# Kernel optimization log

Hardware: AMD Instinct MI355X
Metric: run time of the kernel (lower is better)

The kernel has to match this reference:

```python
import jax, jax.numpy as jnp
import numpy as np

STRIDES = (2, 2, 1)   # module init arg: (2,2,1) per docstring example
EPS = 1e-5            # InstanceNorm epsilon
ALPHA = 0.2           # leaky relu slope
DN = ('NDHWC', 'DHWIO', 'NDHWC')


def setup_inputs() -> dict:
    key = jax.random.key(0)
    k1, k2 = jax.random.split(key, 2)
    # x: [B, D, H, W, Cin] NDHWC volume batch
    x = jax.random.normal(k1, (4, 128, 128, 32, 32), dtype=jnp.float32)
    # w: per-sample hypernetwork kernels [B, kD, kH, kW, Cin, Cout]
    w = jax.random.normal(k2, (4, 3, 3, 3, 32, 64), dtype=jnp.float32) * 0.05
    # InstanceNorm affine params (learned)
    gamma = jnp.ones((64,), dtype=jnp.float32)
    beta = jnp.zeros((64,), dtype=jnp.float32)
    return {"x": x, "w": w, "gamma": gamma, "beta": beta}


def _per_sample_conv(xi, wi):
    # xi: [D,H,W,Cin], wi: [kD,kH,kW,Cin,Cout] -> [D',H',W',Cout]
    return jax.lax.conv_general_dilated(
        xi[None], wi, window_strides=STRIDES, padding='SAME',
        dimension_numbers=DN)[0]


def reference(x, w, gamma, beta):
    # batched dynamic conv: distinct kernel per sample, vectorized via vmap
    y = jax.vmap(_per_sample_conv)(x, w)          # [B, D', H', W', Cout]
    # InstanceNorm: normalize over spatial dims per sample, per channel
    mu = jnp.mean(y, axis=(1, 2, 3), keepdims=True)
    var = jnp.var(y, axis=(1, 2, 3), keepdims=True)
    y = (y - mu) * jax.lax.rsqrt(var + EPS) * gamma + beta
    # leaky relu alpha=0.2
    return jnp.where(y >= 0, y, ALPHA * y)
```

## Files before the change

### kernel.cpp

```cpp
#include <hip/hip_runtime.h>

#define B_ 4
#define D_ 128
#define H_ 128
#define W_ 32
#define CI 32
#define CO 64
#define OD 64
#define OH 64
#define OW 32
#define S_SPATIAL (OD*OH*OW)
#define EPS 1e-5f
#define ALPHA 0.2f

#define XR 9
#define XC 34
#define XUNITS (4*XR*XC)

typedef __attribute__((ext_vector_type(8))) short short8;
typedef __attribute__((ext_vector_type(4))) float f32x4;

__device__ inline short f2bf(float f) {
    union { float f; unsigned u; } v; v.f = f;
    unsigned r = v.u + 0x7FFFu + ((v.u >> 16) & 1u);
    return (short)(r >> 16);
}

__device__ inline short8 pack8(float4 a, float4 b) {
    short8 r;
    r[0]=f2bf(a.x); r[1]=f2bf(a.y); r[2]=f2bf(a.z); r[3]=f2bf(a.w);
    r[4]=f2bf(b.x); r[5]=f2bf(b.y); r[6]=f2bf(b.z); r[7]=f2bf(b.w);
    return r;
}

__global__ __launch_bounds__(512) void zero_ws_kernel(float* ws) {
    ws[threadIdx.x] = 0.f;
}

__global__ __launch_bounds__(64) void wprep_kernel(const float* __restrict__ w,
                                                   short* __restrict__ wp) {
    int blk = blockIdx.x;
    int nf  = blk & 3;
    int tb  = blk >> 2;
    int l   = threadIdx.x;
    int l15 = l & 15, lhi = l >> 4;
    const float* wsrc = w + (size_t)tb * (CI*CO);
    short8 v;
#pragma unroll
    for (int j = 0; j < 8; ++j)
        v[j] = f2bf(wsrc[(lhi*8 + j)*CO + nf*16 + l15]);
    *(short8*)(wp + (size_t)blk*512 + l*8) = v;
}

__global__ __launch_bounds__(256) void conv_mfma_kernel(const float* __restrict__ x,
                                                        const short* __restrict__ wp,
                                                        float* __restrict__ out,
                                                        float* __restrict__ ws) {
    const int bid = blockIdx.x;
    const int b   = bid >> 10;
    const int od  = (bid >> 4) & 63;
    const int oh0 = (bid & 15) << 2;
    const int t   = threadIdx.x;
    const int wv  = t >> 6;
    const int l   = t & 63;
    const int l15 = l & 15;
    const int lhi = l >> 4;

    const float* xb  = x + (size_t)b * (D_*H_*W_*CI);
    const short* wpb = wp + (size_t)b * (27*2048);

    __shared__ short xlds[XUNITS*8];
    __shared__ float lsum[4][64];
    __shared__ float lsq[4][64];

    f32x4 acc[2][4];
#pragma unroll
    for (int mf = 0; mf < 2; ++mf)
#pragma unroll
        for (int nf = 0; nf < 4; ++nf)
            acc[mf][nf] = (f32x4){0.f, 0.f, 0.f, 0.f};

    for (int kd = 0; kd < 3; ++kd) {
        const int id = od*2 + kd;
        if (id >= D_) break;
        const float* xsl = xb + (size_t)id * (H_*W_*CI);

        __syncthreads();
        for (int u = t; u < XUNITS; u += 256) {
            int c  = u % XC;
            int rc = u / XC;
            int r  = rc % XR;
            int g  = rc / XR;
            int ih = oh0*2 + r;
            int iw = c - 1;
            short8 v = (short8){0,0,0,0,0,0,0,0};
            if (ih < H_ && (unsigned)iw < (unsigned)W_) {
                const float* p = xsl + (size_t)ih*(W_*CI) + iw*CI + g*8;
                v = pack8(*(const float4*)p, *(const float4*)(p + 4));
            }
            *(short8*)(xlds + (size_t)u*8) = v;
        }
        __syncthreads();

        const short* wkd = wpb + (size_t)kd*(9*2048) + l*8;
#pragma unroll
        for (int kh = 0; kh < 3; ++kh) {
#pragma unroll
            for (int kw = 0; kw < 3; ++kw) {
                const short* wpt = wkd + (kh*3 + kw)*2048;
                short8 bf0 = *(const short8*)(wpt);
                short8 bf1 = *(const short8*)(wpt + 512);
                short8 bf2 = *(const short8*)(wpt + 1024);
                short8 bf3 = *(const short8*)(wpt + 1536);
                const int r = 2*wv + kh;
#pragma unroll
                for (int mf = 0; mf < 2; ++mf) {
                    int c = mf*16 + l15 + kw;
                    short8 a = *(const short8*)(xlds + (((lhi*XR + r)*XC + c) * 8));
                    acc[mf][0] = __builtin_amdgcn_mfma_f32_16x16x32_bf16(a, bf0, acc[mf][0], 0,0,0);
                    acc[mf][1] = __builtin_amdgcn_mfma_f32_16x16x32_bf16(a, bf1, acc[mf][1], 0,0,0);
                    acc[mf][2] = __builtin_amdgcn_mfma_f32_16x16x32_bf16(a, bf2, acc[mf][2], 0,0,0);
                    acc[mf][3] = __builtin_amdgcn_mfma_f32_16x16x32_bf16(a, bf3, acc[mf][3], 0,0,0);
                }
            }
        }
    }

    const int oh = oh0 + wv;
    float* yb = out + (size_t)((b*OD + od)*OH + oh) * (OW*CO);
#pragma unroll
    for (int mf = 0; mf < 2; ++mf)
#pragma unroll
        for (int nf = 0; nf < 4; ++nf)
#pragma unroll
            for (int r = 0; r < 4; ++r) {
                int ow = mf*16 + lhi*4 + r;
                int co = nf*16 + l15;
                yb[ow*CO + co] = acc[mf][nf][r];
            }

    float csum[4], csq[4];
#pragma unroll
    for (int nf = 0; nf < 4; ++nf) {
        float s = 0.f, q = 0.f;
#pragma unroll
        for (int mf = 0; mf < 2; ++mf)
#pragma unroll
            for (int r = 0; r < 4; ++r) {
                float v = acc[mf][nf][r];
                s += v;
                q = fmaf(v, v, q);
            }
        s += __shfl_xor(s, 16, 64); s += __shfl_xor(s, 32, 64);
        q += __shfl_xor(q, 16, 64); q += __shfl_xor(q, 32, 64);
        csum[nf] = s; csq[nf] = q;
    }
    if (lhi == 0) {
#pragma unroll
        for (int nf = 0; nf < 4; ++nf) {
            lsum[wv][nf*16 + l15] = csum[nf];
            lsq[wv][nf*16 + l15]  = csq[nf];
        }
    }
    __syncthreads();
    if (t < 64) {
        float s = lsum[0][t] + lsum[1][t] + lsum[2][t] + lsum[3][t];
        float q = lsq[0][t]  + lsq[1][t]  + lsq[2][t]  + lsq[3][t];
        atomicAdd(&ws[b*64 + t], s);
        atomicAdd(&ws[256 + b*64 + t], q);
    }
}

__global__ __launch_bounds__(256) void finalize_kernel(float* ws,
                                                       const float* __restrict__ gamma,
                                                       const float* __restrict__ beta) {
    int t = threadIdx.x;
    int co = t & 63;
    const float invS = 1.0f / (float)S_SPATIAL;
    float sum = ws[t];
    float sq  = ws[256 + t];
    float mu  = sum * invS;
    float var = sq * invS - mu*mu;
    float scale = rsqrtf(var + EPS) * gamma[co];
    ws[512 + t] = scale;
    ws[768 + t] = beta[co] - mu*scale;
}

__global__ __launch_bounds__(256) void norm_kernel(float* __restrict__ y,
                                                   const float* __restrict__ ws) {
    size_t i = (size_t)blockIdx.x * 256 + threadIdx.x;
    int b = (int)(i >> 21);
    const float4* scp = (const float4*)(ws + 512 + b*64);
    const float4* shp = (const float4*)(ws + 768 + b*64);
    float4 sc = scp[i & 15];
    float4 sh = shp[i & 15];
    float4 v = ((const float4*)y)[i];
    float4 r;
    r.x = fmaf(v.x, sc.x, sh.x);
    r.y = fmaf(v.y, sc.y, sh.y);
    r.z = fmaf(v.z, sc.z, sh.z);
    r.w = fmaf(v.w, sc.w, sh.w);
    r.x = r.x >= 0.f ? r.x : ALPHA * r.x;
    r.y = r.y >= 0.f ? r.y : ALPHA * r.y;
    r.z = r.z >= 0.f ? r.z : ALPHA * r.z;
    r.w = r.w >= 0.f ? r.w : ALPHA * r.w;
    ((float4*)y)[i] = r;
}

extern "C" void kernel_launch(void* const* d_in, const int* in_sizes, int n_in,
                              void* d_out, int out_size, void* d_ws, size_t ws_size,
                              hipStream_t stream) {
    const float* x     = (const float*)d_in[0];
    const float* w     = (const float*)d_in[1];
    const float* gamma = (const float*)d_in[2];
    const float* beta  = (const float*)d_in[3];
    float* out = (float*)d_out;
    float* ws  = (float*)d_ws;
    short* wp  = (short*)((char*)d_ws + 4096);

    zero_ws_kernel<<<1, 512, 0, stream>>>(ws);
    wprep_kernel<<<B_*27*4, 64, 0, stream>>>(w, wp);
    conv_mfma_kernel<<<B_*OD*(OH/4), 256, 0, stream>>>(x, wp, out, ws);
    finalize_kernel<<<1, 256, 0, stream>>>(ws, gamma, beta);
    norm_kernel<<<32768, 256, 0, stream>>>(out, ws);
}
```

Measured before the change: 239.7 us.

## Stage input slices asynchronously into LDS with double buffering

Replaces the synchronous per-slice global load, bf16 conversion and LDS store with direct global-to-LDS async loads of raw fp32 rows into two swizzled buffers. Loading the next depth slice overlaps with MFMA compute on the current one, and conversion to bf16 moves into the compute loop. Padding is handled by clamping addresses and masking fragments instead of zero-filled halo storage. The cost is doubled LDS use (fp32, two buffers) and repeated per-fragment conversion work, with occupancy hinted at 2 blocks.

```diff
diff --git a/kernel.cpp b/kernel.cpp
--- a/kernel.cpp
+++ b/kernel.cpp
@@ -1,4 +1,5 @@
 #include <hip/hip_runtime.h>
+#include <hip/hip_bf16.h>
 
 #define B_ 4
 #define D_ 128
@@ -13,17 +14,17 @@
 #define EPS 1e-5f
 #define ALPHA 0.2f
 
-#define XR 9
-#define XC 34
-#define XUNITS (4*XR*XC)
+#define XROWS 9
+#define ROWF 1024
+#define SLICEF (XROWS*ROWF)
+#define PLANEF (H_*ROWF)
 
 typedef __attribute__((ext_vector_type(8))) short short8;
 typedef __attribute__((ext_vector_type(4))) float f32x4;
+typedef __attribute__((ext_vector_type(4))) unsigned u32x4;
 
 __device__ inline short f2bf(float f) {
-    union { float f; unsigned u; } v; v.f = f;
-    unsigned r = v.u + 0x7FFFu + ((v.u >> 16) & 1u);
-    return (short)(r >> 16);
+    return __builtin_bit_cast(short, __float2bfloat16(f));
 }
 
 __device__ inline short8 pack8(float4 a, float4 b) {
@@ -31,6 +32,18 @@
     r[0]=f2bf(a.x); r[1]=f2bf(a.y); r[2]=f2bf(a.z); r[3]=f2bf(a.w);
     r[4]=f2bf(b.x); r[5]=f2bf(b.y); r[6]=f2bf(b.z); r[7]=f2bf(b.w);
     return r;
+}
+
+__device__ inline short8 mask_frag(short8 v, unsigned m) {
+    u32x4 u = __builtin_bit_cast(u32x4, v);
+    u[0]&=m; u[1]&=m; u[2]&=m; u[3]&=m;
+    return __builtin_bit_cast(short8, u);
+}
+
+__device__ inline void gload16(const float* g, const float* l) {
+    __builtin_amdgcn_global_load_lds(
+        (const __attribute__((address_space(1))) void*)g,
+        (__attribute__((address_space(3))) void*)l, 16, 0, 0);
 }
 
 __global__ __launch_bounds__(512) void zero_ws_kernel(float* ws) {
@@ -52,10 +65,10 @@
     *(short8*)(wp + (size_t)blk*512 + l*8) = v;
 }
 
-__global__ __launch_bounds__(256) void conv_mfma_kernel(const float* __restrict__ x,
-                                                        const short* __restrict__ wp,
-                                                        float* __restrict__ out,
-                                                        float* __restrict__ ws) {
+__global__ __launch_bounds__(256, 2) void conv_mfma_kernel(const float* __restrict__ x,
+                                                           const short* __restrict__ wp,
+                                                           float* __restrict__ out,
+                                                           float* __restrict__ ws) {
     const int bid = blockIdx.x;
     const int b   = bid >> 10;
     const int od  = (bid >> 4) & 63;
@@ -66,13 +79,26 @@
     const int l15 = l & 15;
     const int lhi = l >> 4;
 
-    const float* xb  = x + (size_t)b * (D_*H_*W_*CI);
+    const float* xb  = x + (size_t)b * (D_*PLANEF);
     const short* wpb = wp + (size_t)b * (27*2048);
 
-    __shared__ short xlds[XUNITS*8];
+    __shared__ __align__(16) float xbuf[2][SLICEF];
     __shared__ float lsum[4][64];
     __shared__ float lsq[4][64];
 
+    const int lnF = (l << 2) ^ ((l & 0x38) >> 1);
+    const int oh02 = oh0 * 2;
+
+    auto stage = [&](const float* xsl, const float* buf) {
+#pragma unroll
+        for (int j = 0; j < 9; ++j) {
+            int s = wv*9 + j;
+            int r = s >> 2, q = s & 3;
+            int ih = oh02 + r; if (ih > H_-1) ih = H_-1;
+            gload16(xsl + (size_t)ih*ROWF + q*256 + lnF, buf + r*ROWF + q*256);
+        }
+    };
+
     f32x4 acc[2][4];
 #pragma unroll
     for (int mf = 0; mf < 2; ++mf)
@@ -80,51 +106,69 @@
         for (int nf = 0; nf < 4; ++nf)
             acc[mf][nf] = (f32x4){0.f, 0.f, 0.f, 0.f};
 
-    for (int kd = 0; kd < 3; ++kd) {
-        const int id = od*2 + kd;
-        if (id >= D_) break;
-        const float* xsl = xb + (size_t)id * (H_*W_*CI);
-
-        __syncthreads();
-        for (int u = t; u < XUNITS; u += 256) {
-            int c  = u % XC;
-            int rc = u / XC;
-            int r  = rc % XR;
-            int g  = rc / XR;
-            int ih = oh0*2 + r;
-            int iw = c - 1;
-            short8 v = (short8){0,0,0,0,0,0,0,0};
-            if (ih < H_ && (unsigned)iw < (unsigned)W_) {
-                const float* p = xsl + (size_t)ih*(W_*CI) + iw*CI + g*8;
-                v = pack8(*(const float4*)p, *(const float4*)(p + 4));
-            }
-            *(short8*)(xlds + (size_t)u*8) = v;
-        }
-        __syncthreads();
-
+    const unsigned mlo = (l15 == 0)  ? 0u : 0xFFFFFFFFu;
+    const unsigned mhi = (l15 == 15) ? 0u : 0xFFFFFFFFu;
+    const int ohw2 = 2*(oh0 + wv);
+
+    auto compute = [&](int kd, const float* buf) {
         const short* wkd = wpb + (size_t)kd*(9*2048) + l*8;
 #pragma unroll
         for (int kh = 0; kh < 3; ++kh) {
-#pragma unroll
-            for (int kw = 0; kw < 3; ++kw) {
-                const short* wpt = wkd + (kh*3 + kw)*2048;
-                short8 bf0 = *(const short8*)(wpt);
-                short8 bf1 = *(const short8*)(wpt + 512);
-                short8 bf2 = *(const short8*)(wpt + 1024);
-                short8 bf3 = *(const short8*)(wpt + 1536);
-                const int r = 2*wv + kh;
-#pragma unroll
-                for (int mf = 0; mf < 2; ++mf) {
-                    int c = mf*16 + l15 + kw;
-                    short8 a = *(const short8*)(xlds + (((lhi*XR + r)*XC + c) * 8));
-                    acc[mf][0] = __builtin_amdgcn_mfma_f32_16x16x32_bf16(a, bf0, acc[mf][0], 0,0,0);
-                    acc[mf][1] = __builtin_amdgcn_mfma_f32_16x16x32_bf16(a, bf1, acc[mf][1], 0,0,0);
-                    acc[mf][2] = __builtin_amdgcn_mfma_f32_16x16x32_bf16(a, bf2, acc[mf][2], 0,0,0);
-                    acc[mf][3] = __builtin_amdgcn_mfma_f32_16x16x32_bf16(a, bf3, acc[mf][3], 0,0,0);
+            short8 bf[3][4];
+#pragma unroll
+            for (int kw = 0; kw < 3; ++kw)
+#pragma unroll
+                for (int nf = 0; nf < 4; ++nf)
+                    bf[kw][nf] = *(const short8*)(wkd + (kh*3 + kw)*2048 + nf*512);
+            if (ohw2 + kh < H_) {
+                const float* pr = buf + (2*wv + kh)*ROWF;
+#pragma unroll
+                for (int kw = 0; kw < 3; ++kw) {
+#pragma unroll
+                    for (int mf = 0; mf < 2; ++mf) {
+                        int iw = mf*16 + l15 + kw - 1;
+                        iw = iw < 0 ? 0 : (iw > 31 ? 31 : iw);
+                        int o  = iw*32 + lhi*8;
+                        int x4 = (iw & 7) << 2;
+                        float4 v0 = *(const float4*)(pr + (o ^ x4));
+                        float4 v1 = *(const float4*)(pr + ((o + 4) ^ x4));
+                        short8 a = pack8(v0, v1);
+                        if (kw == 0 && mf == 0) a = mask_frag(a, mlo);
+                        if (kw == 2 && mf == 1) a = mask_frag(a, mhi);
+                        acc[mf][0] = __builtin_amdgcn_mfma_f32_16x16x32_bf16(a, bf[kw][0], acc[mf][0], 0,0,0);
+                        acc[mf][1] = __builtin_amdgcn_mfma_f32_16x16x32_bf16(a, bf[kw][1], acc[mf][1], 0,0,0);
+                        acc[mf][2] = __builtin_amdgcn_mfma_f32_16x16x32_bf16(a, bf[kw][2], acc[mf][2], 0,0,0);
+                        acc[mf][3] = __builtin_amdgcn_mfma_f32_16x16x32_bf16(a, bf[kw][3], acc[mf][3], 0,0,0);
+                    }
                 }
             }
         }
-    }
+    };
+
+    const int id0 = od*2;
+    const float* xsl0 = xb + (size_t)id0 * PLANEF;
+    const float* xsl1 = xsl0 + PLANEF;
+    int id2c = id0 + 2; if (id2c > D_-1) id2c = D_-1;
+    const float* xsl2 = xb + (size_t)id2c * PLANEF;
+
+    stage(xsl0, xbuf[0]);
+    stage(xsl1, xbuf[1]);
+    asm volatile("s_waitcnt vmcnt(9)" ::: "memory");
+    __builtin_amdgcn_s_barrier();
+    __builtin_amdgcn_sched_barrier(0);
+    compute(0, xbuf[0]);
+    __builtin_amdgcn_s_barrier();
+    __builtin_amdgcn_sched_barrier(0);
+    stage(xsl2, xbuf[0]);
+    asm volatile("s_waitcnt vmcnt(9)" ::: "memory");
+    __builtin_amdgcn_s_barrier();
+    __builtin_amdgcn_sched_barrier(0);
+    compute(1, xbuf[1]);
+    asm volatile("s_waitcnt vmcnt(0)" ::: "memory");
+    __builtin_amdgcn_s_barrier();
+    __builtin_amdgcn_sched_barrier(0);
+    if (id0 + 2 < D_)
+        compute(2, xbuf[0]);
 
     const int oh = oh0 + wv;
     float* yb = out + (size_t)((b*OD + od)*OH + oh) * (OW*CO);
```

Result: faster. 216.6 us (-9.6%).

## Double-buffer input slices in LDS and overlap global loads with MFMA compute

Applied to the files above, without the earlier changes.

Restructures the conv kernel's kd loop into an explicit software pipeline. Input slices go into two LDS buffers, and the next slice's global loads are issued before computing on the current one. Custom barriers wait only on LDS traffic, so vector memory loads stay in flight across barriers. It also precomputes per-thread source offsets, sets launch_bounds occupancy to 4, and uses the library float-to-bf16 conversion. The cost is double the LDS footprint and more registers held across compute, which may limit occupancy.

```diff
diff --git a/kernel.cpp b/kernel.cpp
--- a/kernel.cpp
+++ b/kernel.cpp
@@ -1,4 +1,5 @@
 #include <hip/hip_runtime.h>
+#include <hip/hip_bf16.h>
 
 #define B_ 4
 #define D_ 128
@@ -15,15 +16,15 @@
 
 #define XR 9
 #define XC 34
-#define XUNITS (4*XR*XC)
+#define UNITS (4*XR*XC)
+#define SLICEB (UNITS*16)
+#define PLANEF (H_*W_*CI)
 
 typedef __attribute__((ext_vector_type(8))) short short8;
 typedef __attribute__((ext_vector_type(4))) float f32x4;
 
 __device__ inline short f2bf(float f) {
-    union { float f; unsigned u; } v; v.f = f;
-    unsigned r = v.u + 0x7FFFu + ((v.u >> 16) & 1u);
-    return (short)(r >> 16);
+    return __builtin_bit_cast(short, __float2bfloat16(f));
 }
 
 __device__ inline short8 pack8(float4 a, float4 b) {
@@ -52,10 +53,30 @@
     *(short8*)(wp + (size_t)blk*512 + l*8) = v;
 }
 
-__global__ __launch_bounds__(256) void conv_mfma_kernel(const float* __restrict__ x,
-                                                        const short* __restrict__ wp,
-                                                        float* __restrict__ out,
-                                                        float* __restrict__ ws) {
+#define ISSUE(plane) \
+    _Pragma("unroll") for (int k = 0; k < 5; ++k) { \
+        if (soff[k] >= 0) { \
+            la[k] = *(const float4*)((plane) + soff[k]); \
+            lb[k] = *(const float4*)((plane) + soff[k] + 4); \
+        } else { \
+            la[k] = make_float4(0.f,0.f,0.f,0.f); \
+            lb[k] = la[k]; \
+        } }
+
+#define WRITEB(base) \
+    _Pragma("unroll") for (int k = 0; k < 5; ++k) { \
+        int U_ = t + (k << 8); \
+        if (U_ < UNITS) *(short8*)((base) + U_*16) = pack8(la[k], lb[k]); }
+
+#define BARRIER_KEEP_VMEM() \
+    asm volatile("s_waitcnt lgkmcnt(0)" ::: "memory"); \
+    __builtin_amdgcn_s_barrier(); \
+    __builtin_amdgcn_sched_barrier(0)
+
+__global__ __launch_bounds__(256, 4) void conv_mfma_kernel(const float* __restrict__ x,
+                                                           const short* __restrict__ wp,
+                                                           float* __restrict__ out,
+                                                           float* __restrict__ ws) {
     const int bid = blockIdx.x;
     const int b   = bid >> 10;
     const int od  = (bid >> 4) & 63;
@@ -66,12 +87,26 @@
     const int l15 = l & 15;
     const int lhi = l >> 4;
 
-    const float* xb  = x + (size_t)b * (D_*H_*W_*CI);
+    const float* xb  = x + (size_t)b * (D_*PLANEF);
     const short* wpb = wp + (size_t)b * (27*2048);
 
-    __shared__ short xlds[XUNITS*8];
-    __shared__ float lsum[4][64];
-    __shared__ float lsq[4][64];
+    __shared__ __align__(16) char smem[2*SLICEB];
+    char* buf0 = smem;
+    char* buf1 = smem + SLICEB;
+
+    int soff[5];
+#pragma unroll
+    for (int k = 0; k < 5; ++k) {
+        int U   = t + (k << 8);
+        int g   = U / (XR*XC);
+        int rem = U % (XR*XC);
+        int r   = rem / XC;
+        int c   = rem % XC;
+        int ih  = oh0*2 + r;
+        int iw  = c - 1;
+        soff[k] = (U < UNITS && ih < H_ && (unsigned)iw < (unsigned)W_)
+                    ? (ih*(W_*CI) + iw*CI + g*8) : -1;
+    }
 
     f32x4 acc[2][4];
 #pragma unroll
@@ -80,31 +115,11 @@
         for (int nf = 0; nf < 4; ++nf)
             acc[mf][nf] = (f32x4){0.f, 0.f, 0.f, 0.f};
 
-    for (int kd = 0; kd < 3; ++kd) {
-        const int id = od*2 + kd;
-        if (id >= D_) break;
-        const float* xsl = xb + (size_t)id * (H_*W_*CI);
-
-        __syncthreads();
-        for (int u = t; u < XUNITS; u += 256) {
-            int c  = u % XC;
-            int rc = u / XC;
-            int r  = rc % XR;
-            int g  = rc / XR;
-            int ih = oh0*2 + r;
-            int iw = c - 1;
-            short8 v = (short8){0,0,0,0,0,0,0,0};
-            if (ih < H_ && (unsigned)iw < (unsigned)W_) {
-                const float* p = xsl + (size_t)ih*(W_*CI) + iw*CI + g*8;
-                v = pack8(*(const float4*)p, *(const float4*)(p + 4));
-            }
-            *(short8*)(xlds + (size_t)u*8) = v;
-        }
-        __syncthreads();
-
+    auto compute = [&](int kd, const char* base) {
         const short* wkd = wpb + (size_t)kd*(9*2048) + l*8;
 #pragma unroll
         for (int kh = 0; kh < 3; ++kh) {
+            const int r = 2*wv + kh;
 #pragma unroll
             for (int kw = 0; kw < 3; ++kw) {
                 const short* wpt = wkd + (kh*3 + kw)*2048;
@@ -112,11 +127,11 @@
                 short8 bf1 = *(const short8*)(wpt + 512);
                 short8 bf2 = *(const short8*)(wpt + 1024);
                 short8 bf3 = *(const short8*)(wpt + 1536);
-                const int r = 2*wv + kh;
 #pragma unroll
                 for (int mf = 0; mf < 2; ++mf) {
                     int c = mf*16 + l15 + kw;
-                    short8 a = *(const short8*)(xlds + (((lhi*XR + r)*XC + c) * 8));
+                    int U = (lhi*XR + r)*XC + c;
+                    short8 a = *(const short8*)(base + U*16);
                     acc[mf][0] = __builtin_amdgcn_mfma_f32_16x16x32_bf16(a, bf0, acc[mf][0], 0,0,0);
                     acc[mf][1] = __builtin_amdgcn_mfma_f32_16x16x32_bf16(a, bf1, acc[mf][1], 0,0,0);
                     acc[mf][2] = __builtin_amdgcn_mfma_f32_16x16x32_bf16(a, bf2, acc[mf][2], 0,0,0);
@@ -124,7 +139,32 @@
                 }
             }
         }
-    }
+    };
+
+    const int id0 = od*2;
+    const float* p0 = xb + (size_t)id0 * PLANEF;
+    const float* p1 = p0 + PLANEF;
+    const bool has2 = (id0 + 2) < D_;
+    const float* p2 = has2 ? (p1 + PLANEF) : p1;
+
+    float4 la[5], lb[5];
+
+    ISSUE(p0);
+    WRITEB(buf0);
+    ISSUE(p1);
+    BARRIER_KEEP_VMEM();
+
+    compute(0, buf0);
+    WRITEB(buf1);
+    BARRIER_KEEP_VMEM();
+
+    ISSUE(p2);
+    __builtin_amdgcn_sched_barrier(0);
+    compute(1, buf1);
+    WRITEB(buf0);
+    BARRIER_KEEP_VMEM();
+
+    if (has2) compute(2, buf0);
 
     const int oh = oh0 + wv;
     float* yb = out + (size_t)((b*OD + od)*OH + oh) * (OW*CO);
@@ -139,6 +179,9 @@
                 yb[ow*CO + co] = acc[mf][nf][r];
             }
 
+    __syncthreads();
+    float* lsum = (float*)smem;
+    float* lsq  = (float*)(smem + 1024);
     float csum[4], csq[4];
 #pragma unroll
     for (int nf = 0; nf < 4; ++nf) {
@@ -158,14 +201,14 @@
     if (lhi == 0) {
 #pragma unroll
         for (int nf = 0; nf < 4; ++nf) {
-            lsum[wv][nf*16 + l15] = csum[nf];
-            lsq[wv][nf*16 + l15]  = csq[nf];
+            lsum[wv*64 + nf*16 + l15] = csum[nf];
+            lsq[wv*64 + nf*16 + l15]  = csq[nf];
         }
     }
     __syncthreads();
     if (t < 64) {
-        float s = lsum[0][t] + lsum[1][t] + lsum[2][t] + lsum[3][t];
-        float q = lsq[0][t]  + lsq[1][t]  + lsq[2][t]  + lsq[3][t];
+        float s = lsum[t] + lsum[64 + t] + lsum[128 + t] + lsum[192 + t];
+        float q = lsq[t]  + lsq[64 + t]  + lsq[128 + t]  + lsq[192 + t];
         atomicAdd(&ws[b*64 + t], s);
         atomicAdd(&ws[256 + b*64 + t], q);
     }
```

New measurement: 247.3 us. 3.2% more time.
